# Kernel optimization log

Hardware: AMD Instinct MI355X
Metric: run time of the kernel (lower is better)

Reference implementation:

```python
import jax, jax.numpy as jnp
import numpy as np

N, E, D, T = 100000, 1600000, 128, 5
EPS = 1e-5


def setup_inputs() -> dict:
    key = jax.random.key(0)
    ks = jax.random.split(key, 8)
    scale = 1.0 / np.sqrt(D)
    return {
        "features": jax.random.normal(ks[0], (N, D), dtype=jnp.float32),
        "src": jax.random.randint(ks[1], (E,), 0, N, dtype=jnp.int32),
        "dst": jax.random.randint(ks[2], (E,), 0, N, dtype=jnp.int32),
        "etype": jax.random.randint(ks[3], (E,), 0, T, dtype=jnp.int32),
        "w1": jax.random.normal(ks[4], (T * D, D), dtype=jnp.float32) * scale,
        "b1": jnp.zeros((T * D,), dtype=jnp.float32),
        "g1": jnp.ones((D,), dtype=jnp.float32),
        "be1": jnp.zeros((D,), dtype=jnp.float32),
        "w2": jax.random.normal(ks[5], (T * D, D), dtype=jnp.float32) * scale,
        "b2": jnp.zeros((T * D,), dtype=jnp.float32),
        "g2": jnp.ones((D,), dtype=jnp.float32),
        "be2": jnp.zeros((D,), dtype=jnp.float32),
    }


def _bn(x, gamma, beta):
    # BatchNorm1d in training mode: biased batch statistics over node axis.
    mu = jnp.mean(x, axis=0)
    var = jnp.mean((x - mu) ** 2, axis=0)
    return gamma * (x - mu) * jax.lax.rsqrt(var + EPS) + beta


def _round(x, w, b, gamma, beta, src, dst, etype):
    h = jax.nn.relu(_bn(x, gamma, beta))
    h = jnp.einsum('nd,od->no', h, w) + b          # [N, T*D]
    h3 = h.reshape(N, T, D)
    # one-hot multiply + sum over types == select the etype slice per edge
    msg = h3[src, etype]                            # [E, D] gather
    return jax.ops.segment_sum(msg, dst, num_segments=N)  # [N, D] scatter-add


def reference(features, src, dst, etype, w1, b1, g1, be1, w2, b2, g2, be2):
    h_new = _round(features, w1, b1, g1, be1, src, dst, etype)
    h_new = _round(h_new, w2, b2, g2, be2, src, dst, etype)
    return h_new + features
```

## Files before the change

### kernel.cpp

```cpp
#include <hip/hip_runtime.h>

#define NN 100000
#define EE 1600000
#define DD 128
#define TD 640
#define EPSV 1e-5f
#define NBLK_SCAN 391
#define SB 1024
#define NRANGE 8
#define RSZ 12500
#define NCHUNK 256
#define CSZ 6250

typedef __attribute__((ext_vector_type(8))) short bf16x8;
typedef __attribute__((ext_vector_type(4))) float f32x4;

__device__ inline unsigned short f2b(float f) {
  union { float f; unsigned u; } x; x.f = f;
  unsigned r = x.u + 0x7fff + ((x.u >> 16) & 1);
  return (unsigned short)(r >> 16);
}
__device__ inline float b2f(unsigned short u) {
  union { unsigned u; float f; } x; x.u = ((unsigned)u) << 16;
  return x.f;
}

__global__ __launch_bounds__(256) void k_stats_partial(const float* __restrict__ x,
    float* __restrict__ ps, float* __restrict__ pq) {
  float s0=0.f,s1=0.f,s2=0.f,s3=0.f,q0=0.f,q1=0.f,q2=0.f,q3=0.f;
  const float4* x4 = reinterpret_cast<const float4*>(x);
  const int total = NN * DD / 4;
  for (int i = blockIdx.x * 256 + threadIdx.x; i < total; i += SB * 256) {
    float4 v = x4[i];
    s0 += v.x; s1 += v.y; s2 += v.z; s3 += v.w;
    q0 += v.x*v.x; q1 += v.y*v.y; q2 += v.z*v.z; q3 += v.w*v.w;
  }
  __shared__ float ls[256], lq[256];
  int t = threadIdx.x;
  float sv[4] = {s0,s1,s2,s3}, qv[4] = {q0,q1,q2,q3};
#pragma unroll
  for (int j = 0; j < 4; ++j) {
    ls[t] = sv[j]; lq[t] = qv[j];
    __syncthreads();
    if (t < 32) {
      float a = 0.f, b = 0.f;
#pragma unroll
      for (int k = 0; k < 8; ++k) { a += ls[t + 32*k]; b += lq[t + 32*k]; }
      ps[blockIdx.x * DD + t*4 + j] = a;
      pq[blockIdx.x * DD + t*4 + j] = b;
    }
    __syncthreads();
  }
}

__global__ __launch_bounds__(1024) void k_stats_final(const float* __restrict__ ps,
    const float* __restrict__ pq, const float* __restrict__ g,
    const float* __restrict__ be, float* __restrict__ ssb) {
  __shared__ float ls[1024], lq[1024];
  int t = threadIdx.x;
  int col = t & 127, seg = t >> 7;
  float s = 0.f, q = 0.f;
  for (int b = seg; b < SB; b += 8) { s += ps[b * DD + col]; q += pq[b * DD + col]; }
  ls[t] = s; lq[t] = q;
  __syncthreads();
  if (t < 128) {
#pragma unroll
    for (int k = 1; k < 8; ++k) { s += ls[t + 128*k]; q += lq[t + 128*k]; }
    float mean = s * (1.0f / NN);
    float var  = q * (1.0f / NN) - mean * mean;
    float sc = g[t] * rsqrtf(var + EPSV);
    ssb[t] = sc;
    ssb[DD + t] = be[t] - mean * sc;
  }
}

__global__ __launch_bounds__(256) void k_act(const float* __restrict__ x,
    const float* __restrict__ ss, unsigned short* __restrict__ A) {
  int i = blockIdx.x * 256 + threadIdx.x;
  float4 v = reinterpret_cast<const float4*>(x)[i];
  int c4 = (i & 31) * 4;
  float s0 = ss[c4+0], s1 = ss[c4+1], s2 = ss[c4+2], s3 = ss[c4+3];
  float h0 = ss[DD+c4+0], h1 = ss[DD+c4+1], h2 = ss[DD+c4+2], h3 = ss[DD+c4+3];
  ushort4 o;
  o.x = f2b(fmaxf(0.f, v.x * s0 + h0));
  o.y = f2b(fmaxf(0.f, v.y * s1 + h1));
  o.z = f2b(fmaxf(0.f, v.z * s2 + h2));
  o.w = f2b(fmaxf(0.f, v.w * s3 + h3));
  reinterpret_cast<ushort4*>(A)[i] = o;
}

__global__ void k_cvt(const float* __restrict__ w, unsigned short* __restrict__ o) {
  int i = blockIdx.x * 256 + threadIdx.x;
  float4 v = reinterpret_cast<const float4*>(w)[i];
  ushort4 u; u.x = f2b(v.x); u.y = f2b(v.y); u.z = f2b(v.z); u.w = f2b(v.w);
  reinterpret_cast<ushort4*>(o)[i] = u;
}

__global__ void k_zero(int* p, int n) {
  int i = blockIdx.x * 256 + threadIdx.x;
  if (i < n) p[i] = 0;
}
__global__ __launch_bounds__(256) void k_hist(const int* __restrict__ dst,
    int* __restrict__ cnt) {
  const int range = blockIdx.x & (NRANGE - 1);
  const int chunk = blockIdx.x >> 3;
  const int lo = range * RSZ;
  const int base = chunk * CSZ;
  for (int i = base + threadIdx.x; i < base + CSZ; i += 256) {
    int d = dst[i];
    if ((unsigned)(d - lo) < RSZ) atomicAdd(&cnt[d], 1);
  }
}
__global__ __launch_bounds__(256) void k_scan_blk(const int* __restrict__ cnt, int* __restrict__ bsum) {
  __shared__ int sh[256];
  int idx = blockIdx.x * 256 + threadIdx.x;
  sh[threadIdx.x] = (idx < NN) ? cnt[idx] : 0;
  __syncthreads();
  for (int off = 128; off > 0; off >>= 1) {
    if (threadIdx.x < off) sh[threadIdx.x] += sh[threadIdx.x + off];
    __syncthreads();
  }
  if (threadIdx.x == 0) bsum[blockIdx.x] = sh[0];
}
__global__ __launch_bounds__(512) void k_scan_top(int* __restrict__ bsum) {
  __shared__ int sh[512];
  int t = threadIdx.x;
  int v = (t < NBLK_SCAN) ? bsum[t] : 0;
  sh[t] = v;
  __syncthreads();
  for (int off = 1; off < 512; off <<= 1) {
    int add = (t >= off) ? sh[t - off] : 0;
    __syncthreads();
    sh[t] += add;
    __syncthreads();
  }
  if (t < NBLK_SCAN) bsum[t] = sh[t] - v;
}
__global__ __launch_bounds__(256) void k_scan_fin(const int* __restrict__ cnt,
    const int* __restrict__ bsum, int* __restrict__ row_ptr, int* __restrict__ cursor) {
  __shared__ int sh[256];
  int idx = blockIdx.x * 256 + threadIdx.x;
  int v = (idx < NN) ? cnt[idx] : 0;
  sh[threadIdx.x] = v;
  __syncthreads();
  for (int off = 1; off < 256; off <<= 1) {
    int add = (threadIdx.x >= off) ? sh[threadIdx.x - off] : 0;
    __syncthreads();
    sh[threadIdx.x] += add;
    __syncthreads();
  }
  int excl = bsum[blockIdx.x] + sh[threadIdx.x] - v;
  if (idx < NN) { row_ptr[idx] = excl; cursor[idx] = excl; }
  if (idx == NN - 1) row_ptr[NN] = excl + v;
}
__global__ __launch_bounds__(256) void k_scatter(const int* __restrict__ src,
    const int* __restrict__ dst, const int* __restrict__ et,
    int* __restrict__ cursor, int* __restrict__ payload) {
  const int range = blockIdx.x & (NRANGE - 1);
  const int chunk = blockIdx.x >> 3;
  const int lo = range * RSZ;
  const int base = chunk * CSZ;
  for (int i = base + threadIdx.x; i < base + CSZ; i += 256) {
    int d = dst[i];
    if ((unsigned)(d - lo) < RSZ) {
      int pos = atomicAdd(&cursor[d], 1);
      payload[pos] = (src[i] << 3) | et[i];
    }
  }
}

__global__ __launch_bounds__(256) void k_gemm(const unsigned short* __restrict__ A,
    const unsigned short* __restrict__ W, const float* __restrict__ bias,
    unsigned short* __restrict__ H) {
  __shared__ unsigned short wlds[2][8192];
  const int t = threadIdx.x;
  const int l = t & 63;
  const int w = t >> 6;
  const int lm = l & 15;
  const int hi = l >> 4;
  const int R = blockIdx.x * 64 + w * 16;

  int arow = R + lm; if (arow >= NN) arow = NN - 1;
  const unsigned short* aptr = A + arow * DD + hi * 8;
  bf16x8 af[4];
#pragma unroll
  for (int kk = 0; kk < 4; ++kk)
    af[kk] = *reinterpret_cast<const bf16x8*>(aptr + kk * 32);

#pragma unroll
  for (int k = 0; k < 4; ++k) {
    int i = k * 256 + t;
    int r = i >> 4, b = (i & 15) * 16;
    float4 v = *reinterpret_cast<const float4*>(
        reinterpret_cast<const char*>(W) + r * 256 + b);
    *reinterpret_cast<float4*>(
        reinterpret_cast<char*>(wlds[0]) + r * 256 + (b ^ ((r & 7) << 4))) = v;
  }
  __syncthreads();

  const int r0 = R + hi * 4;
#pragma unroll 1
  for (int cb = 0; cb < 10; ++cb) {
    const int buf = cb & 1;
    if (cb < 9) {
#pragma unroll
      for (int k = 0; k < 4; ++k) {
        int i = k * 256 + t;
        int r = i >> 4, b = (i & 15) * 16;
        float4 v = *reinterpret_cast<const float4*>(
            reinterpret_cast<const char*>(W) + ((cb + 1) * 64 + r) * 256 + b);
        *reinterpret_cast<float4*>(
            reinterpret_cast<char*>(wlds[buf ^ 1]) + r * 256 + (b ^ ((r & 7) << 4))) = v;
      }
    }
    f32x4 acc[4] = {};
#pragma unroll
    for (int kk = 0; kk < 4; ++kk) {
#pragma unroll
      for (int f = 0; f < 4; ++f) {
        int rr = f * 16 + lm;
        bf16x8 bfr = *reinterpret_cast<const bf16x8*>(
            reinterpret_cast<char*>(wlds[buf]) + rr * 256 +
            ((kk * 64 + hi * 16) ^ ((rr & 7) << 4)));
        acc[f] = __builtin_amdgcn_mfma_f32_16x16x32_bf16(af[kk], bfr, acc[f], 0, 0, 0);
      }
    }
#pragma unroll
    for (int f = 0; f < 4; ++f) {
      int col = cb * 64 + f * 16 + lm;
      float bv = bias[col];
#pragma unroll
      for (int r = 0; r < 4; ++r) {
        int row = r0 + r;
        if (row < NN) H[row * TD + col] = f2b(acc[f][r] + bv);
      }
    }
    __syncthreads();
  }
}

__global__ __launch_bounds__(256) void k_gather(const unsigned short* __restrict__ H,
    const int* __restrict__ rp, const int* __restrict__ pl,
    const float* __restrict__ base, float* __restrict__ y) {
  int m = blockIdx.x * 4 + (threadIdx.x >> 6);
  int l = threadIdx.x & 63;
  int s = rp[m], e = rp[m + 1];
  float a0 = 0.f, a1 = 0.f;
  if (base) {
    float2 b = reinterpret_cast<const float2*>(base)[m * 64 + l];
    a0 = b.x; a1 = b.y;
  }
  int j = s;
  for (; j + 1 < e; j += 2) {
    int p0 = pl[j], p1 = pl[j + 1];
    ushort2 u0 = reinterpret_cast<const ushort2*>(H + (p0 >> 3) * TD + (p0 & 7) * DD)[l];
    ushort2 u1 = reinterpret_cast<const ushort2*>(H + (p1 >> 3) * TD + (p1 & 7) * DD)[l];
    a0 += b2f(u0.x) + b2f(u1.x);
    a1 += b2f(u0.y) + b2f(u1.y);
  }
  if (j < e) {
    int p0 = pl[j];
    ushort2 u0 = reinterpret_cast<const ushort2*>(H + (p0 >> 3) * TD + (p0 & 7) * DD)[l];
    a0 += b2f(u0.x);
    a1 += b2f(u0.y);
  }
  float2 o; o.x = a0; o.y = a1;
  reinterpret_cast<float2*>(y)[m * 64 + l] = o;
}

extern "C" void kernel_launch(void* const* d_in, const int* in_sizes, int n_in,
                              void* d_out, int out_size, void* d_ws, size_t ws_size,
                              hipStream_t stream) {
  const float* features = (const float*)d_in[0];
  const int*   src   = (const int*)d_in[1];
  const int*   dst   = (const int*)d_in[2];
  const int*   etype = (const int*)d_in[3];
  const float* w1  = (const float*)d_in[4];
  const float* b1  = (const float*)d_in[5];
  const float* g1  = (const float*)d_in[6];
  const float* be1 = (const float*)d_in[7];
  const float* w2  = (const float*)d_in[8];
  const float* b2  = (const float*)d_in[9];
  const float* g2  = (const float*)d_in[10];
  const float* be2 = (const float*)d_in[11];

  char* ws = (char*)d_ws;
  unsigned short* Ab   = (unsigned short*)(ws + 0);
  float*          ps   = (float*)(ws + 0);
  float*          pq   = (float*)(ws + 524288);
  unsigned short* Hb   = (unsigned short*)(ws + 25600000);
  float*          y1   = (float*)(ws + 153600000);
  unsigned short* w1b  = (unsigned short*)(ws + 204800000);
  unsigned short* w2b  = (unsigned short*)(ws + 204963840);
  float*          ssb  = (float*)(ws + 205127680);
  int*            rowp = (int*)(ws + 205390848);
  int*            curs = (int*)(ws + 205790864);
  int*            payl = (int*)(ws + 206190864);
  int*            bsum = (int*)(ws + 212590864);

  k_zero<<<(NN + 255) / 256, 256, 0, stream>>>(curs, NN);
  k_hist<<<NRANGE * NCHUNK, 256, 0, stream>>>(dst, curs);
  k_scan_blk<<<NBLK_SCAN, 256, 0, stream>>>(curs, bsum);
  k_scan_top<<<1, 512, 0, stream>>>(bsum);
  k_scan_fin<<<NBLK_SCAN, 256, 0, stream>>>(curs, bsum, rowp, curs);
  k_scatter<<<NRANGE * NCHUNK, 256, 0, stream>>>(src, dst, etype, curs, payl);

  k_cvt<<<80, 256, 0, stream>>>(w1, w1b);
  k_cvt<<<80, 256, 0, stream>>>(w2, w2b);

  k_stats_partial<<<SB, 256, 0, stream>>>(features, ps, pq);
  k_stats_final<<<1, 1024, 0, stream>>>(ps, pq, g1, be1, ssb);
  k_act<<<12500, 256, 0, stream>>>(features, ssb, Ab);
  k_gemm<<<1563, 256, 0, stream>>>(Ab, w1b, b1, Hb);
  k_gather<<<NN / 4, 256, 0, stream>>>(Hb, rowp, payl, nullptr, y1);

  k_stats_partial<<<SB, 256, 0, stream>>>(y1, ps, pq);
  k_stats_final<<<1, 1024, 0, stream>>>(ps, pq, g2, be2, ssb);
  k_act<<<12500, 256, 0, stream>>>(y1, ssb, Ab);
  k_gemm<<<1563, 256, 0, stream>>>(Ab, w2b, b2, Hb);
  k_gather<<<NN / 4, 256, 0, stream>>>(Hb, rowp, payl, features, (float*)d_out);
}
```

Measured before the change: 629.0 us.

## Aggregate per-type neighbor features before GEMM instead of gathering transformed rows

Reorders each round as aggregate-then-transform. Per destination node it sums the bf16 activations of source nodes into five per-type buckets plus per-type edge counts, then runs one GEMM with K=640 against rearranged weights and adds count-weighted biases. This removes the gather of 640-wide transformed rows and the large H intermediate, since the gather now reads 128-wide activation rows and the GEMM output is only 128 wide. The intermediate y1 is also stored as bf16, which halves its traffic but adds rounding error to the second round's batch statistics.

```diff
diff --git a/kernel.cpp b/kernel.cpp
--- a/kernel.cpp
+++ b/kernel.cpp
@@ -34,6 +34,35 @@
     float4 v = x4[i];
     s0 += v.x; s1 += v.y; s2 += v.z; s3 += v.w;
     q0 += v.x*v.x; q1 += v.y*v.y; q2 += v.z*v.z; q3 += v.w*v.w;
+  }
+  __shared__ float ls[256], lq[256];
+  int t = threadIdx.x;
+  float sv[4] = {s0,s1,s2,s3}, qv[4] = {q0,q1,q2,q3};
+#pragma unroll
+  for (int j = 0; j < 4; ++j) {
+    ls[t] = sv[j]; lq[t] = qv[j];
+    __syncthreads();
+    if (t < 32) {
+      float a = 0.f, b = 0.f;
+#pragma unroll
+      for (int k = 0; k < 8; ++k) { a += ls[t + 32*k]; b += lq[t + 32*k]; }
+      ps[blockIdx.x * DD + t*4 + j] = a;
+      pq[blockIdx.x * DD + t*4 + j] = b;
+    }
+    __syncthreads();
+  }
+}
+
+__global__ __launch_bounds__(256) void k_stats_partial_bf(const unsigned short* __restrict__ x,
+    float* __restrict__ ps, float* __restrict__ pq) {
+  float s0=0.f,s1=0.f,s2=0.f,s3=0.f,q0=0.f,q1=0.f,q2=0.f,q3=0.f;
+  const ushort4* x4 = reinterpret_cast<const ushort4*>(x);
+  const int total = NN * DD / 4;
+  for (int i = blockIdx.x * 256 + threadIdx.x; i < total; i += SB * 256) {
+    ushort4 u = x4[i];
+    float vx = b2f(u.x), vy = b2f(u.y), vz = b2f(u.z), vw = b2f(u.w);
+    s0 += vx; s1 += vy; s2 += vz; s3 += vw;
+    q0 += vx*vx; q1 += vy*vy; q2 += vz*vz; q3 += vw*vw;
   }
   __shared__ float ls[256], lq[256];
   int t = threadIdx.x;
@@ -89,11 +118,29 @@
   reinterpret_cast<ushort4*>(A)[i] = o;
 }
 
-__global__ void k_cvt(const float* __restrict__ w, unsigned short* __restrict__ o) {
+__global__ __launch_bounds__(256) void k_act_bf(const unsigned short* __restrict__ x,
+    const float* __restrict__ ss, unsigned short* __restrict__ A) {
   int i = blockIdx.x * 256 + threadIdx.x;
+  ushort4 u = reinterpret_cast<const ushort4*>(x)[i];
+  int c4 = (i & 31) * 4;
+  float s0 = ss[c4+0], s1 = ss[c4+1], s2 = ss[c4+2], s3 = ss[c4+3];
+  float h0 = ss[DD+c4+0], h1 = ss[DD+c4+1], h2 = ss[DD+c4+2], h3 = ss[DD+c4+3];
+  ushort4 o;
+  o.x = f2b(fmaxf(0.f, b2f(u.x) * s0 + h0));
+  o.y = f2b(fmaxf(0.f, b2f(u.y) * s1 + h1));
+  o.z = f2b(fmaxf(0.f, b2f(u.z) * s2 + h2));
+  o.w = f2b(fmaxf(0.f, b2f(u.w) * s3 + h3));
+  reinterpret_cast<ushort4*>(A)[i] = o;
+}
+
+__global__ void k_cvt_b2(const float* __restrict__ w, unsigned short* __restrict__ o) {
+  int i = blockIdx.x * 256 + threadIdx.x;
+  int tt = i >> 12;
+  int rem = i & 4095;
+  int d = rem >> 5, j = rem & 31;
   float4 v = reinterpret_cast<const float4*>(w)[i];
   ushort4 u; u.x = f2b(v.x); u.y = f2b(v.y); u.z = f2b(v.z); u.w = f2b(v.w);
-  reinterpret_cast<ushort4*>(o)[i] = u;
+  reinterpret_cast<ushort4*>(o)[d * 160 + tt * 32 + j] = u;
 }
 
 __global__ void k_zero(int* p, int n) {
@@ -169,9 +216,66 @@
   }
 }
 
-__global__ __launch_bounds__(256) void k_gemm(const unsigned short* __restrict__ A,
-    const unsigned short* __restrict__ W, const float* __restrict__ bias,
-    unsigned short* __restrict__ H) {
+__global__ __launch_bounds__(256) void k_agg(const unsigned short* __restrict__ Ab,
+    const int* __restrict__ rp, const int* __restrict__ pl,
+    unsigned short* __restrict__ G, int* __restrict__ cntb) {
+  const int n = blockIdx.x * 4 + (threadIdx.x >> 6);
+  const int l = threadIdx.x & 63;
+  const int s = rp[n], e = rp[n + 1];
+  float a00=0.f,a01=0.f,a10=0.f,a11=0.f,a20=0.f,a21=0.f,a30=0.f,a31=0.f,a40=0.f,a41=0.f;
+  int c0=0,c1=0,c2=0,c3=0,c4=0;
+  int j = s;
+  for (; j + 1 < e; j += 2) {
+    int p0 = pl[j], p1 = pl[j + 1];
+    ushort2 u0 = *reinterpret_cast<const ushort2*>(Ab + (p0 >> 3) * DD + 2 * l);
+    ushort2 u1 = *reinterpret_cast<const ushort2*>(Ab + (p1 >> 3) * DD + 2 * l);
+    float x0 = b2f(u0.x), x1 = b2f(u0.y);
+    switch (p0 & 7) {
+      case 0: a00 += x0; a01 += x1; c0++; break;
+      case 1: a10 += x0; a11 += x1; c1++; break;
+      case 2: a20 += x0; a21 += x1; c2++; break;
+      case 3: a30 += x0; a31 += x1; c3++; break;
+      default: a40 += x0; a41 += x1; c4++; break;
+    }
+    float z0 = b2f(u1.x), z1 = b2f(u1.y);
+    switch (p1 & 7) {
+      case 0: a00 += z0; a01 += z1; c0++; break;
+      case 1: a10 += z0; a11 += z1; c1++; break;
+      case 2: a20 += z0; a21 += z1; c2++; break;
+      case 3: a30 += z0; a31 += z1; c3++; break;
+      default: a40 += z0; a41 += z1; c4++; break;
+    }
+  }
+  if (j < e) {
+    int p0 = pl[j];
+    ushort2 u0 = *reinterpret_cast<const ushort2*>(Ab + (p0 >> 3) * DD + 2 * l);
+    float x0 = b2f(u0.x), x1 = b2f(u0.y);
+    switch (p0 & 7) {
+      case 0: a00 += x0; a01 += x1; c0++; break;
+      case 1: a10 += x0; a11 += x1; c1++; break;
+      case 2: a20 += x0; a21 += x1; c2++; break;
+      case 3: a30 += x0; a31 += x1; c3++; break;
+      default: a40 += x0; a41 += x1; c4++; break;
+    }
+  }
+  unsigned short* gp = G + n * TD + 2 * l;
+  ushort2 o;
+  o.x = f2b(a00); o.y = f2b(a01); *reinterpret_cast<ushort2*>(gp + 0 * DD) = o;
+  o.x = f2b(a10); o.y = f2b(a11); *reinterpret_cast<ushort2*>(gp + 1 * DD) = o;
+  o.x = f2b(a20); o.y = f2b(a21); *reinterpret_cast<ushort2*>(gp + 2 * DD) = o;
+  o.x = f2b(a30); o.y = f2b(a31); *reinterpret_cast<ushort2*>(gp + 3 * DD) = o;
+  o.x = f2b(a40); o.y = f2b(a41); *reinterpret_cast<ushort2*>(gp + 4 * DD) = o;
+  if (l < 5) {
+    int c = (l == 0) ? c0 : (l == 1) ? c1 : (l == 2) ? c2 : (l == 3) ? c3 : c4;
+    cntb[n * 8 + l] = c;
+  }
+}
+
+template<int RND>
+__global__ __launch_bounds__(256) void k_gemm2(const unsigned short* __restrict__ G,
+    const unsigned short* __restrict__ B2, const float* __restrict__ bias,
+    const int* __restrict__ cntb, const float* __restrict__ base,
+    void* __restrict__ out) {
   __shared__ unsigned short wlds[2][8192];
   const int t = threadIdx.x;
   const int l = t & 63;
@@ -181,91 +285,77 @@
   const int R = blockIdx.x * 64 + w * 16;
 
   int arow = R + lm; if (arow >= NN) arow = NN - 1;
-  const unsigned short* aptr = A + arow * DD + hi * 8;
-  bf16x8 af[4];
-#pragma unroll
-  for (int kk = 0; kk < 4; ++kk)
-    af[kk] = *reinterpret_cast<const bf16x8*>(aptr + kk * 32);
+  const unsigned short* aptr = G + arow * TD + hi * 8;
 
 #pragma unroll
   for (int k = 0; k < 4; ++k) {
-    int i = k * 256 + t;
-    int r = i >> 4, b = (i & 15) * 16;
+    int idx = k * 256 + t;
+    int c = idx >> 3, sub = idx & 7;
     float4 v = *reinterpret_cast<const float4*>(
-        reinterpret_cast<const char*>(W) + r * 256 + b);
+        reinterpret_cast<const char*>(B2) + c * 1280 + sub * 16);
     *reinterpret_cast<float4*>(
-        reinterpret_cast<char*>(wlds[0]) + r * 256 + (b ^ ((r & 7) << 4))) = v;
+        reinterpret_cast<char*>(wlds[0]) + c * 128 + ((sub * 16) ^ ((c & 7) << 4))) = v;
   }
   __syncthreads();
 
+  f32x4 acc[8] = {};
+#pragma unroll 1
+  for (int ks = 0; ks < 10; ++ks) {
+    const int buf = ks & 1;
+    if (ks < 9) {
+#pragma unroll
+      for (int k = 0; k < 4; ++k) {
+        int idx = k * 256 + t;
+        int c = idx >> 3, sub = idx & 7;
+        float4 v = *reinterpret_cast<const float4*>(
+            reinterpret_cast<const char*>(B2) + c * 1280 + (ks + 1) * 128 + sub * 16);
+        *reinterpret_cast<float4*>(
+            reinterpret_cast<char*>(wlds[buf ^ 1]) + c * 128 + ((sub * 16) ^ ((c & 7) << 4))) = v;
+      }
+    }
+    bf16x8 af0 = *reinterpret_cast<const bf16x8*>(aptr + ks * 64);
+    bf16x8 af1 = *reinterpret_cast<const bf16x8*>(aptr + ks * 64 + 32);
+#pragma unroll
+    for (int f = 0; f < 8; ++f) {
+      int rr = f * 16 + lm;
+      bf16x8 b0 = *reinterpret_cast<const bf16x8*>(
+          reinterpret_cast<char*>(wlds[buf]) + rr * 128 + ((hi * 16) ^ ((rr & 7) << 4)));
+      bf16x8 b1 = *reinterpret_cast<const bf16x8*>(
+          reinterpret_cast<char*>(wlds[buf]) + rr * 128 + ((64 + hi * 16) ^ ((rr & 7) << 4)));
+      acc[f] = __builtin_amdgcn_mfma_f32_16x16x32_bf16(af0, b0, acc[f], 0, 0, 0);
+      acc[f] = __builtin_amdgcn_mfma_f32_16x16x32_bf16(af1, b1, acc[f], 0, 0, 0);
+    }
+    __syncthreads();
+  }
+
   const int r0 = R + hi * 4;
-#pragma unroll 1
-  for (int cb = 0; cb < 10; ++cb) {
-    const int buf = cb & 1;
-    if (cb < 9) {
-#pragma unroll
-      for (int k = 0; k < 4; ++k) {
-        int i = k * 256 + t;
-        int r = i >> 4, b = (i & 15) * 16;
-        float4 v = *reinterpret_cast<const float4*>(
-            reinterpret_cast<const char*>(W) + ((cb + 1) * 64 + r) * 256 + b);
-        *reinterpret_cast<float4*>(
-            reinterpret_cast<char*>(wlds[buf ^ 1]) + r * 256 + (b ^ ((r & 7) << 4))) = v;
+  float cn[4][5];
+#pragma unroll
+  for (int r = 0; r < 4; ++r) {
+    int row = r0 + r; if (row >= NN) row = NN - 1;
+#pragma unroll
+    for (int tt = 0; tt < 5; ++tt) cn[r][tt] = (float)cntb[row * 8 + tt];
+  }
+#pragma unroll
+  for (int f = 0; f < 8; ++f) {
+    int col = f * 16 + lm;
+    float bb0 = bias[col], bb1 = bias[128 + col], bb2 = bias[256 + col],
+          bb3 = bias[384 + col], bb4 = bias[512 + col];
+#pragma unroll
+    for (int r = 0; r < 4; ++r) {
+      int row = r0 + r;
+      if (row < NN) {
+        float v = acc[f][r] + cn[r][0]*bb0 + cn[r][1]*bb1 + cn[r][2]*bb2
+                            + cn[r][3]*bb3 + cn[r][4]*bb4;
+        if (RND == 1) {
+          v += base[row * DD + col];
+          reinterpret_cast<float*>(out)[row * DD + col] = v;
+        } else {
+          reinterpret_cast<unsigned short*>(out)[row * DD + col] = f2b(v);
+        }
       }
     }
-    f32x4 acc[4] = {};
-#pragma unroll
-    for (int kk = 0; kk < 4; ++kk) {
-#pragma unroll
-      for (int f = 0; f < 4; ++f) {
-        int rr = f * 16 + lm;
-        bf16x8 bfr = *reinterpret_cast<const bf16x8*>(
-            reinterpret_cast<char*>(wlds[buf]) + rr * 256 +
-            ((kk * 64 + hi * 16) ^ ((rr & 7) << 4)));
-        acc[f] = __builtin_amdgcn_mfma_f32_16x16x32_bf16(af[kk], bfr, acc[f], 0, 0, 0);
-      }
-    }
-#pragma unroll
-    for (int f = 0; f < 4; ++f) {
-      int col = cb * 64 + f * 16 + lm;
-      float bv = bias[col];
-#pragma unroll
-      for (int r = 0; r < 4; ++r) {
-        int row = r0 + r;
-        if (row < NN) H[row * TD + col] = f2b(acc[f][r] + bv);
-      }
-    }
-    __syncthreads();
-  }
-}
-
-__global__ __launch_bounds__(256) void k_gather(const unsigned short* __restrict__ H,
-    const int* __restrict__ rp, const int* __restrict__ pl,
-    const float* __restrict__ base, float* __restrict__ y) {
-  int m = blockIdx.x * 4 + (threadIdx.x >> 6);
-  int l = threadIdx.x & 63;
-  int s = rp[m], e = rp[m + 1];
-  float a0 = 0.f, a1 = 0.f;
-  if (base) {
-    float2 b = reinterpret_cast<const float2*>(base)[m * 64 + l];
-    a0 = b.x; a1 = b.y;
-  }
-  int j = s;
-  for (; j + 1 < e; j += 2) {
-    int p0 = pl[j], p1 = pl[j + 1];
-    ushort2 u0 = reinterpret_cast<const ushort2*>(H + (p0 >> 3) * TD + (p0 & 7) * DD)[l];
-    ushort2 u1 = reinterpret_cast<const ushort2*>(H + (p1 >> 3) * TD + (p1 & 7) * DD)[l];
-    a0 += b2f(u0.x) + b2f(u1.x);
-    a1 += b2f(u0.y) + b2f(u1.y);
-  }
-  if (j < e) {
-    int p0 = pl[j];
-    ushort2 u0 = reinterpret_cast<const ushort2*>(H + (p0 >> 3) * TD + (p0 & 7) * DD)[l];
-    a0 += b2f(u0.x);
-    a1 += b2f(u0.y);
-  }
-  float2 o; o.x = a0; o.y = a1;
-  reinterpret_cast<float2*>(y)[m * 64 + l] = o;
+  }
 }
 
 extern "C" void kernel_launch(void* const* d_in, const int* in_sizes, int n_in,
@@ -288,15 +378,16 @@
   unsigned short* Ab   = (unsigned short*)(ws + 0);
   float*          ps   = (float*)(ws + 0);
   float*          pq   = (float*)(ws + 524288);
-  unsigned short* Hb   = (unsigned short*)(ws + 25600000);
-  float*          y1   = (float*)(ws + 153600000);
-  unsigned short* w1b  = (unsigned short*)(ws + 204800000);
-  unsigned short* w2b  = (unsigned short*)(ws + 204963840);
-  float*          ssb  = (float*)(ws + 205127680);
-  int*            rowp = (int*)(ws + 205390848);
-  int*            curs = (int*)(ws + 205790864);
-  int*            payl = (int*)(ws + 206190864);
-  int*            bsum = (int*)(ws + 212590864);
+  unsigned short* G    = (unsigned short*)(ws + 25600000);
+  unsigned short* y1   = (unsigned short*)(ws + 153600000);
+  unsigned short* b2a  = (unsigned short*)(ws + 179200000);
+  unsigned short* b2b  = (unsigned short*)(ws + 179363840);
+  float*          ssb  = (float*)(ws + 179527680);
+  int*            rowp = (int*)(ws + 179528704);
+  int*            curs = (int*)(ws + 179928720);
+  int*            payl = (int*)(ws + 180328720);
+  int*            bsum = (int*)(ws + 186728720);
+  int*            cntb = (int*)(ws + 186730768);
 
   k_zero<<<(NN + 255) / 256, 256, 0, stream>>>(curs, NN);
   k_hist<<<NRANGE * NCHUNK, 256, 0, stream>>>(dst, curs);
@@ -305,18 +396,18 @@
   k_scan_fin<<<NBLK_SCAN, 256, 0, stream>>>(curs, bsum, rowp, curs);
   k_scatter<<<NRANGE * NCHUNK, 256, 0, stream>>>(src, dst, etype, curs, payl);
 
-  k_cvt<<<80, 256, 0, stream>>>(w1, w1b);
-  k_cvt<<<80, 256, 0, stream>>>(w2, w2b);
+  k_cvt_b2<<<80, 256, 0, stream>>>(w1, b2a);
+  k_cvt_b2<<<80, 256, 0, stream>>>(w2, b2b);
 
   k_stats_partial<<<SB, 256, 0, stream>>>(features, ps, pq);
   k_stats_final<<<1, 1024, 0, stream>>>(ps, pq, g1, be1, ssb);
   k_act<<<12500, 256, 0, stream>>>(features, ssb, Ab);
-  k_gemm<<<1563, 256, 0, stream>>>(Ab, w1b, b1, Hb);
-  k_gather<<<NN / 4, 256, 0, stream>>>(Hb, rowp, payl, nullptr, y1);
-
-  k_stats_partial<<<SB, 256, 0, stream>>>(y1, ps, pq);
+  k_agg<<<NN / 4, 256, 0, stream>>>(Ab, rowp, payl, G, cntb);
+  k_gemm2<0><<<1563, 256, 0, stream>>>(G, b2a, b1, cntb, nullptr, y1);
+
+  k_stats_partial_bf<<<SB, 256, 0, stream>>>(y1, ps, pq);
   k_stats_final<<<1, 1024, 0, stream>>>(ps, pq, g2, be2, ssb);
-  k_act<<<12500, 256, 0, stream>>>(y1, ssb, Ab);
-  k_gemm<<<1563, 256, 0, stream>>>(Ab, w2b, b2, Hb);
-  k_gather<<<NN / 4, 256, 0, stream>>>(Hb, rowp, payl, features, (float*)d_out);
-}
+  k_act_bf<<<12500, 256, 0, stream>>>(y1, ssb, Ab);
+  k_agg<<<NN / 4, 256, 0, stream>>>(Ab, rowp, payl, G, cntb);
+  k_gemm2<1><<<1563, 256, 0, stream>>>(G, b2b, b2, cntb, features, d_out);
+}
```

Measured after the change: 610.7 us. 1.03x faster.
